# Optimization experiments

Hardware: AMD Instinct MI355X
Metric: run time of the kernel (lower is better)

Reference implementation:

```python
import jax, jax.numpy as jnp
import numpy as np

# dims: episodes E, steps S, comm length L, hidden H, rnn input IN, comm vocab OUT
E, S, L, H, IN, OUT = 64, 32, 32, 1024, 2048, 64
TAU = 2.0      # MTRNN leaky-integrator time constant
EPS = 1e-5     # BatchNorm eps


def setup_inputs() -> dict:
    key = jax.random.key(0)
    ks = jax.random.split(key, 16)
    def p(k, shape, scale=0.02):
        return jax.random.normal(k, shape, jnp.float32) * scale
    return {
        "h_w_action": jax.random.normal(ks[0], (E, S, IN), jnp.float32),
        # MTRNN cell
        "Wx": p(ks[1], (IN, H)), "bx": jnp.zeros((H,), jnp.float32),
        "Wh": p(ks[2], (H, H)), "bh": jnp.zeros((H,), jnp.float32),
        # Ted_Conv1d: 4 branches, kernels 1/3/5/7, each H//4 out channels (OIH layout)
        "w1": p(ks[3], (H // 4, H, 1)), "b1": jnp.zeros((H // 4,), jnp.float32),
        "w3": p(ks[4], (H // 4, H, 3)), "b3": jnp.zeros((H // 4,), jnp.float32),
        "w5": p(ks[5], (H // 4, H, 5)), "b5": jnp.zeros((H // 4,), jnp.float32),
        "w7": p(ks[6], (H // 4, H, 7)), "b7": jnp.zeros((H // 4,), jnp.float32),
        # BatchNorm1d affine
        "gamma": jnp.ones((H,), jnp.float32), "beta": jnp.zeros((H,), jnp.float32),
        # PReLU (single shared slope, torch default init 0.25)
        "prelu_a": jnp.array(0.25, jnp.float32),
        # output Linear
        "Wout": p(ks[7], (H, OUT)), "bout": jnp.zeros((OUT,), jnp.float32),
    }


def _conv(x, w, b):
    # x: [N, C, L], w: [O, I, k], 'same' padding for odd kernels
    pad = (w.shape[-1] - 1) // 2
    y = jax.lax.conv_general_dilated(x, w, (1,), [(pad, pad)],
                                     dimension_numbers=('NCH', 'OIH', 'NCH'))
    return y + b[None, :, None]


def reference(h_w_action, Wx, bx, Wh, bh, w1, b1, w3, b3, w5, b5, w7, b7,
              gamma, beta, prelu_a, Wout, bout):
    # MTRNN: same input every step; leaky integration h' = (1-1/tau)h + (1/tau)tanh(Wx x + Wh h)
    x_r = h_w_action @ Wx + bx                      # [E,S,H], constant across steps
    h0 = jnp.zeros((E, S, H), h_w_action.dtype)

    def step(h, _):
        h_new = (1.0 - 1.0 / TAU) * h + (1.0 / TAU) * jnp.tanh(x_r + h @ Wh + bh)
        return h_new, h_new

    _, hs = jax.lax.scan(step, h0, None, length=L)  # [L,E,S,H]
    hs = hs.transpose(1, 2, 0, 3).reshape(E * S, L, H)

    # multi-kernel conv over the comm-length axis
    xc = hs.transpose(0, 2, 1)                      # [N,H,L]
    y = jnp.concatenate([_conv(xc, w1, b1), _conv(xc, w3, b3),
                         _conv(xc, w5, b5), _conv(xc, w7, b7)], axis=1)  # [N,H,L]

    # BatchNorm1d (training-mode batch stats over N and L), affine
    mean = y.mean(axis=(0, 2), keepdims=True)
    var = y.var(axis=(0, 2), keepdims=True)
    y = (y - mean) * jax.lax.rsqrt(var + EPS) * gamma[None, :, None] + beta[None, :, None]

    # PReLU; Dropout is identity at eval
    y = jnp.where(y > 0, y, prelu_a * y)

    y = y.transpose(0, 2, 1).reshape(E, S, L, H)
    return y @ Wout + bout                          # [E,S,L,OUT]
```

## Files before the change

### kernel.cpp

```cpp
#include <hip/hip_runtime.h>
#include <cstdint>
#include <cmath>

#define DI __device__ __forceinline__


typedef __attribute__((ext_vector_type(8))) short bf16x8;
typedef __attribute__((ext_vector_type(4))) short s16x4;
typedef __attribute__((ext_vector_type(4))) float f32x4;

DI float bf2f(short u){
  union { unsigned int i; float f; } v; v.i = ((unsigned int)(unsigned short)u) << 16; return v.f;
}
DI short f2bf(float f){
  unsigned int x = __builtin_bit_cast(unsigned int, f);
  unsigned int r = (x + 0x7FFFu + ((x >> 16) & 1u)) >> 16;
  return (short)(unsigned short)r;
}
DI void gload16(const void* g, void* l){
  __builtin_amdgcn_global_load_lds(
      (const __attribute__((address_space(1))) unsigned int*)g,
      (__attribute__((address_space(3))) unsigned int*)l, 16, 0, 0);
}

template<int BM, int BN, int MODE>
__global__ __launch_bounds__(256)
void gemm_k(const short* __restrict__ A, long lda,
            const short* __restrict__ Bt, long ldb, int Ksteps,
            const float* __restrict__ bias,
            float* __restrict__ f32out,
            const float* __restrict__ f32in,
            short* __restrict__ bfout, int jj)
{
  constexpr int WTM = BM / 2, WTN = BN / 2;
  constexpr int FM = WTM / 16, FN = WTN / 16;
  __shared__ short As[BM * 64];
  __shared__ short Bs[BN * 64];
  const int tid = threadIdx.x;
  const int w = tid >> 6, l = tid & 63;
  const int wr = w >> 1, wc = w & 1;
  const int lr = l & 15, lk = (l >> 4) << 3;
  const int brow = blockIdx.x * BM;
  const int bcol = blockIdx.y * BN;

  int coff = 0, jout = 0;
  if constexpr (MODE == 2) {
    const int bb = bcol >> 7;
    const int dlt = (bb < 2) ? -3 : (bb < 6) ? -2 : (bb < 12) ? -1
                  : (bb < 20) ? 0 : (bb < 26) ? 1 : (bb < 30) ? 2 : 3;
    coff = (dlt == -3) ? 768 : (dlt == -2) ? 256 : (dlt == -1) ? -512
         : (dlt == 0) ? -1536 : (dlt == 1) ? -2304 : (dlt == 2) ? -2816 : -3072;
    jout = jj - dlt;
    if (jout < 0 || jout > 31) return;
  }

  f32x4 acc[FM][FN];
  #pragma unroll
  for (int i = 0; i < FM; i++)
    #pragma unroll
    for (int j = 0; j < FN; j++) {
      acc[i][j][0] = 0.f; acc[i][j][1] = 0.f; acc[i][j][2] = 0.f; acc[i][j][3] = 0.f;
    }

  for (int ks = 0; ks < Ksteps; ++ks) {
    const short* ab = A + (long)brow * lda + (long)ks * 64;
    #pragma unroll
    for (int it = 0; it < BM / 32; ++it) {
      int ci = it * 256 + tid;
      gload16(ab + (long)(ci >> 3) * lda + ((ci & 7) << 3),
              As + ((it * 256 + (w << 6)) << 3));
    }
    const short* bb2 = Bt + (long)bcol * ldb + (long)ks * 64;
    #pragma unroll
    for (int it = 0; it < BN / 32; ++it) {
      int ci = it * 256 + tid;
      gload16(bb2 + (long)(ci >> 3) * ldb + ((ci & 7) << 3),
              Bs + ((it * 256 + (w << 6)) << 3));
    }
    __syncthreads();
    #pragma unroll
    for (int kk = 0; kk < 64; kk += 32) {
      bf16x8 a[FM], b[FN];
      #pragma unroll
      for (int i = 0; i < FM; i++)
        a[i] = *(const bf16x8*)&As[(wr * WTM + i * 16 + lr) * 64 + kk + lk];
      #pragma unroll
      for (int j = 0; j < FN; j++)
        b[j] = *(const bf16x8*)&Bs[(wc * WTN + j * 16 + lr) * 64 + kk + lk];
      #pragma unroll
      for (int i = 0; i < FM; i++)
        #pragma unroll
        for (int j = 0; j < FN; j++)
          acc[i][j] = __builtin_amdgcn_mfma_f32_16x16x32_bf16(a[i], b[j], acc[i][j], 0, 0, 0);
    }
    __syncthreads();
  }

  const int rbase = brow + wr * WTM;
  const int cbase = bcol + wc * WTN;
  const int rl = (l >> 4) << 2;
  #pragma unroll
  for (int i = 0; i < FM; i++) {
    #pragma unroll
    for (int j = 0; j < FN; j++) {
      #pragma unroll
      for (int r = 0; r < 4; r++) {
        const int row = rbase + i * 16 + rl + r;
        const int col = cbase + j * 16 + lr;
        const float v = acc[i][j][r];
        if constexpr (MODE == 0) {
          f32out[(long)row * 1024 + col] = v + bias[col];
        } else if constexpr (MODE == 1) {
          const long idx = (long)row * 1024 + col;
          const float hn = 0.5f * f32out[idx] + 0.5f * tanhf(f32in[idx] + v + bias[col]);
          f32out[idx] = hn;
          bfout[idx] = f2bf(hn);
        } else if constexpr (MODE == 2) {
          short* yp = bfout + ((long)row * 32 + jout) * 1024 + (col + coff);
          *yp = f2bf(bf2f(*yp) + v);
        } else {
          f32out[(long)row * 64 + col] = v + bias[col];
        }
      }
    }
  }
}

__global__ void zero16(float4* __restrict__ p, long n)
{
  long i = (long)blockIdx.x * 256 + threadIdx.x;
  if (i < n) p[i] = float4{0.f, 0.f, 0.f, 0.f};
}

__global__ void cvt4_f32_bf16(const float* __restrict__ in, short* __restrict__ out, int n4)
{
  int i = blockIdx.x * 256 + threadIdx.x;
  if (i >= n4) return;
  float4 v = ((const float4*)in)[i];
  s16x4 o; o[0] = f2bf(v.x); o[1] = f2bf(v.y); o[2] = f2bf(v.z); o[3] = f2bf(v.w);
  ((s16x4*)out)[i] = o;
}

__global__ void transpose_f32_bf16(const float* __restrict__ in, short* __restrict__ out,
                                   int R, int C)
{
  __shared__ short tile[32][33];
  const int tx = threadIdx.x & 31, ty = threadIdx.x >> 5;
  const int c0 = blockIdx.x * 32, r0 = blockIdx.y * 32;
  #pragma unroll
  for (int i = 0; i < 32; i += 8)
    tile[ty + i][tx] = f2bf(in[(long)(r0 + ty + i) * C + (c0 + tx)]);
  __syncthreads();
  #pragma unroll
  for (int i = 0; i < 32; i += 8)
    out[(long)(c0 + ty + i) * R + (r0 + tx)] = tile[tx][ty + i];
}

__global__ void build_wpack(const float* __restrict__ w1, const float* __restrict__ w3,
                            const float* __restrict__ w5, const float* __restrict__ w7,
                            short* __restrict__ Wp)
{
  const int pc = blockIdx.x;
  int dlt, c;
  if      (pc < 256)  { dlt = -3; c = pc + 768; }
  else if (pc < 768)  { dlt = -2; c = pc + 256; }
  else if (pc < 1536) { dlt = -1; c = pc - 512; }
  else if (pc < 2560) { dlt = 0;  c = pc - 1536; }
  else if (pc < 3328) { dlt = 1;  c = pc - 2304; }
  else if (pc < 3840) { dlt = 2;  c = pc - 2816; }
  else                { dlt = 3;  c = pc - 3072; }
  const int b = c >> 8, kb = 2 * b + 1, t = dlt + b, oo = c & 255;
  const float* w = (b == 0) ? w1 : (b == 1) ? w3 : (b == 2) ? w5 : w7;
  short* dst = Wp + (long)pc * 1024;
  for (int i = threadIdx.x; i < 1024; i += 256)
    dst[i] = f2bf(w[((long)oo * 1024 + i) * kb + t]);
}

__global__ void bn_stats(const short* __restrict__ y, float* __restrict__ sum,
                         float* __restrict__ ssq)
{
  const int c0 = threadIdx.x * 4;
  float s0 = 0, s1 = 0, s2 = 0, s3 = 0, q0 = 0, q1 = 0, q2 = 0, q3 = 0;
  const long base = (long)blockIdx.x * 256;
  for (int r = 0; r < 256; ++r) {
    s16x4 v = *(const s16x4*)(y + (base + r) * 1024 + c0);
    float f0 = bf2f(v[0]), f1 = bf2f(v[1]), f2v = bf2f(v[2]), f3 = bf2f(v[3]);
    s0 += f0; s1 += f1; s2 += f2v; s3 += f3;
    q0 += f0 * f0; q1 += f1 * f1; q2 += f2v * f2v; q3 += f3 * f3;
  }
  atomicAdd(&sum[c0 + 0], s0); atomicAdd(&sum[c0 + 1], s1);
  atomicAdd(&sum[c0 + 2], s2); atomicAdd(&sum[c0 + 3], s3);
  atomicAdd(&ssq[c0 + 0], q0); atomicAdd(&ssq[c0 + 1], q1);
  atomicAdd(&ssq[c0 + 2], q2); atomicAdd(&ssq[c0 + 3], q3);
}

__global__ void bn_finalize(const float* __restrict__ bnsum, const float* __restrict__ bnss,
                            const float* __restrict__ gamma, const float* __restrict__ beta,
                            float* __restrict__ scale, float* __restrict__ shift)
{
  int c = blockIdx.x * 256 + threadIdx.x;
  const float inv = 1.f / 65536.f;
  float mean = bnsum[c] * inv;
  float var = bnss[c] * inv - mean * mean;
  float sc = gamma[c] * rsqrtf(var + 1e-5f);
  scale[c] = sc;
  shift[c] = beta[c] - mean * sc;
}

__global__ void bn_apply(short* __restrict__ y, const float* __restrict__ scale,
                         const float* __restrict__ shift, const float* __restrict__ aP)
{
  const float a = *aP;
  long i = (long)blockIdx.x * 256 + threadIdx.x;
  s16x4 v = ((s16x4*)y)[i];
  int c0 = (int)((i * 4) & 1023);
  #pragma unroll
  for (int j = 0; j < 4; ++j) {
    float f = bf2f(v[j]) * scale[c0 + j] + shift[c0 + j];
    f = f > 0.f ? f : a * f;
    v[j] = f2bf(f);
  }
  ((s16x4*)y)[i] = v;
}

extern "C" void kernel_launch(void* const* d_in, const int* in_sizes, int n_in,
                              void* d_out, int out_size, void* d_ws, size_t ws_size,
                              hipStream_t stream)
{
  const float* h_w_action = (const float*)d_in[0];
  const float* Wx   = (const float*)d_in[1];
  const float* bx   = (const float*)d_in[2];
  const float* Wh   = (const float*)d_in[3];
  const float* bh   = (const float*)d_in[4];
  const float* w1   = (const float*)d_in[5];
  const float* w3   = (const float*)d_in[7];
  const float* w5   = (const float*)d_in[9];
  const float* w7   = (const float*)d_in[11];
  const float* gamma = (const float*)d_in[13];
  const float* beta  = (const float*)d_in[14];
  const float* prelu = (const float*)d_in[15];
  const float* Wout  = (const float*)d_in[16];
  const float* bout  = (const float*)d_in[17];
  float* out = (float*)d_out;

  char* p = (char*)d_ws;
  auto alloc = [&](size_t bytes) -> char* {
    char* r = p; p += (bytes + 255) & ~(size_t)255; return r;
  };
  short* y     = (short*)alloc(65536L * 1024 * 2);
  float* xr    = (float*)alloc(2048L * 1024 * 4);
  float* hf    = (float*)alloc(2048L * 1024 * 4);
  short* hb0   = (short*)alloc(2048L * 1024 * 2);
  short* hb1   = (short*)alloc(2048L * 1024 * 2);
  short* A1    = (short*)alloc(2048L * 2048 * 2);
  short* WxT   = (short*)alloc(1024L * 2048 * 2);
  short* WhT   = (short*)alloc(1024L * 1024 * 2);
  short* Wp    = (short*)alloc(4096L * 1024 * 2);
  short* WoutT = (short*)alloc(64L * 1024 * 2);
  float* bnsum = (float*)alloc(1024 * 4);
  float* bnss  = (float*)alloc(1024 * 4);
  float* scal  = (float*)alloc(1024 * 4);
  float* shft  = (float*)alloc(1024 * 4);

  if ((size_t)(p - (char*)d_ws) > ws_size) return;

  zero16<<<32768, 256, 0, stream>>>((float4*)y, 65536L * 1024 * 2 / 16);
  zero16<<<2048, 256, 0, stream>>>((float4*)hf, 2048L * 1024 * 4 / 16);
  zero16<<<1024, 256, 0, stream>>>((float4*)hb0, 2048L * 1024 * 2 / 16);
  zero16<<<1, 256, 0, stream>>>((float4*)bnsum, 256);
  zero16<<<1, 256, 0, stream>>>((float4*)bnss, 256);

  cvt4_f32_bf16<<<4096, 256, 0, stream>>>(h_w_action, A1, 2048 * 2048 / 4);
  transpose_f32_bf16<<<dim3(32, 64), 256, 0, stream>>>(Wx, WxT, 2048, 1024);
  transpose_f32_bf16<<<dim3(32, 32), 256, 0, stream>>>(Wh, WhT, 1024, 1024);
  transpose_f32_bf16<<<dim3(2, 32), 256, 0, stream>>>(Wout, WoutT, 1024, 64);
  build_wpack<<<4096, 256, 0, stream>>>(w1, w3, w5, w7, Wp);

  gemm_k<128, 128, 0><<<dim3(16, 8), 256, 0, stream>>>(
      A1, 2048, WxT, 2048, 32, bx, xr, nullptr, nullptr, 0);

  short* hb[2] = {hb0, hb1};
  for (int s = 1; s <= 32; ++s) {
    gemm_k<64, 128, 1><<<dim3(32, 8), 256, 0, stream>>>(
        hb[(s - 1) & 1], 1024, WhT, 1024, 16, bh, hf, xr, hb[s & 1], 0);
    gemm_k<128, 128, 2><<<dim3(16, 32), 256, 0, stream>>>(
        hb[s & 1], 1024, Wp, 1024, 16, nullptr, nullptr, nullptr, y, s - 1);
  }

  bn_stats<<<256, 256, 0, stream>>>(y, bnsum, bnss);
  bn_finalize<<<4, 256, 0, stream>>>(bnsum, bnss, gamma, beta, scal, shft);
  bn_apply<<<65536, 256, 0, stream>>>(y, scal, shft, prelu);

  gemm_k<128, 64, 3><<<dim3(512, 1), 256, 0, stream>>>(
      y, 1024, WoutT, 1024, 16, bout, out, nullptr, nullptr, 0);
}
```

Baseline: 2.136 ms.

## Fuse BN apply and PReLU into output GEMM, retile GEMMs, precompute load pointers

Drops the separate bn_apply pass over the 128MB bf16 activation buffer. The output GEMM now applies the BatchNorm scale/shift and PReLU while staging A tiles into LDS, which saves a full read and write of y. It also increases bn_stats parallelism, shrinks the tiles of the input projection and recurrent GEMMs to launch more blocks, and hoists the global load pointer arithmetic out of the K loop. The fused kernel uses register loads for A instead of direct-to-LDS loads, which may add latency in the output GEMM.

```diff
diff --git a/kernel.cpp b/kernel.cpp
--- a/kernel.cpp
+++ b/kernel.cpp
@@ -34,6 +34,7 @@
 {
   constexpr int WTM = BM / 2, WTN = BN / 2;
   constexpr int FM = WTM / 16, FN = WTN / 16;
+  constexpr int AIT = BM / 32, BIT = BN / 32;
   __shared__ short As[BM * 64];
   __shared__ short Bs[BN * 64];
   const int tid = threadIdx.x;
@@ -62,20 +63,27 @@
       acc[i][j][0] = 0.f; acc[i][j][1] = 0.f; acc[i][j][2] = 0.f; acc[i][j][3] = 0.f;
     }
 
+  const short* ap[AIT];
+  const short* bp[BIT];
+  const int rsub = tid >> 3;
+  const int koff = (tid & 7) << 3;
+  #pragma unroll
+  for (int it = 0; it < AIT; ++it)
+    ap[it] = A + (long)(brow + it * 32 + rsub) * lda + koff;
+  #pragma unroll
+  for (int it = 0; it < BIT; ++it)
+    bp[it] = Bt + (long)(bcol + it * 32 + rsub) * ldb + koff;
+
   for (int ks = 0; ks < Ksteps; ++ks) {
-    const short* ab = A + (long)brow * lda + (long)ks * 64;
-    #pragma unroll
-    for (int it = 0; it < BM / 32; ++it) {
-      int ci = it * 256 + tid;
-      gload16(ab + (long)(ci >> 3) * lda + ((ci & 7) << 3),
-              As + ((it * 256 + (w << 6)) << 3));
-    }
-    const short* bb2 = Bt + (long)bcol * ldb + (long)ks * 64;
-    #pragma unroll
-    for (int it = 0; it < BN / 32; ++it) {
-      int ci = it * 256 + tid;
-      gload16(bb2 + (long)(ci >> 3) * ldb + ((ci & 7) << 3),
-              Bs + ((it * 256 + (w << 6)) << 3));
+    #pragma unroll
+    for (int it = 0; it < AIT; ++it) {
+      gload16(ap[it], As + ((it * 256 + (w << 6)) << 3));
+      ap[it] += 64;
+    }
+    #pragma unroll
+    for (int it = 0; it < BIT; ++it) {
+      gload16(bp[it], Bs + ((it * 256 + (w << 6)) << 3));
+      bp[it] += 64;
     }
     __syncthreads();
     #pragma unroll
@@ -126,6 +134,94 @@
   }
 }
 
+__global__ __launch_bounds__(256)
+void g5_bn(const short* __restrict__ y, const short* __restrict__ WoutT,
+           const float* __restrict__ scal, const float* __restrict__ shft,
+           const float* __restrict__ aP, const float* __restrict__ bout,
+           float* __restrict__ out)
+{
+  __shared__ short As[128 * 64];
+  __shared__ short Bs[64 * 64];
+  __shared__ float sS[1024], sB[1024];
+  const int tid = threadIdx.x;
+  const int w = tid >> 6, l = tid & 63;
+  const int wr = w >> 1, wc = w & 1;
+  const int lr = l & 15, lk = (l >> 4) << 3;
+  const int m0 = blockIdx.x * 128;
+  for (int i = tid; i < 1024; i += 256) { sS[i] = scal[i]; sB[i] = shft[i]; }
+  const float a = *aP;
+  __syncthreads();
+
+  f32x4 acc[4][2];
+  #pragma unroll
+  for (int i = 0; i < 4; i++)
+    #pragma unroll
+    for (int j = 0; j < 2; j++) {
+      acc[i][j][0] = 0.f; acc[i][j][1] = 0.f; acc[i][j][2] = 0.f; acc[i][j][3] = 0.f;
+    }
+
+  const int rsub = tid >> 3;
+  const int koff = (tid & 7) << 3;
+  const short* yp[4];
+  #pragma unroll
+  for (int it = 0; it < 4; ++it)
+    yp[it] = y + (long)(m0 + it * 32 + rsub) * 1024 + koff;
+  const short* bp[2];
+  #pragma unroll
+  for (int it = 0; it < 2; ++it)
+    bp[it] = WoutT + (long)(it * 32 + rsub) * 1024 + koff;
+
+  for (int ks = 0; ks < 16; ++ks) {
+    #pragma unroll
+    for (int it = 0; it < 2; ++it) {
+      gload16(bp[it], Bs + ((it * 256 + (w << 6)) << 3));
+      bp[it] += 64;
+    }
+    const int c0 = ks * 64 + koff;
+    #pragma unroll
+    for (int it = 0; it < 4; ++it) {
+      bf16x8 v = *(const bf16x8*)yp[it];
+      yp[it] += 64;
+      #pragma unroll
+      for (int e = 0; e < 8; ++e) {
+        float f = bf2f(v[e]) * sS[c0 + e] + sB[c0 + e];
+        v[e] = f2bf(f > 0.f ? f : a * f);
+      }
+      *(bf16x8*)(As + ((it * 256 + tid) << 3)) = v;
+    }
+    __syncthreads();
+    #pragma unroll
+    for (int kk = 0; kk < 64; kk += 32) {
+      bf16x8 af[4], bf_[2];
+      #pragma unroll
+      for (int i = 0; i < 4; i++)
+        af[i] = *(const bf16x8*)&As[(wr * 64 + i * 16 + lr) * 64 + kk + lk];
+      #pragma unroll
+      for (int j = 0; j < 2; j++)
+        bf_[j] = *(const bf16x8*)&Bs[(wc * 32 + j * 16 + lr) * 64 + kk + lk];
+      #pragma unroll
+      for (int i = 0; i < 4; i++)
+        #pragma unroll
+        for (int j = 0; j < 2; j++)
+          acc[i][j] = __builtin_amdgcn_mfma_f32_16x16x32_bf16(af[i], bf_[j], acc[i][j], 0, 0, 0);
+    }
+    __syncthreads();
+  }
+
+  const int rbase = m0 + wr * 64, cbase = wc * 32;
+  const int rl = (l >> 4) << 2;
+  #pragma unroll
+  for (int i = 0; i < 4; i++)
+    #pragma unroll
+    for (int j = 0; j < 2; j++)
+      #pragma unroll
+      for (int r = 0; r < 4; r++) {
+        const int row = rbase + i * 16 + rl + r;
+        const int col = cbase + j * 16 + lr;
+        out[(long)row * 64 + col] = acc[i][j][r] + bout[col];
+      }
+}
+
 __global__ void zero16(float4* __restrict__ p, long n)
 {
   long i = (long)blockIdx.x * 256 + threadIdx.x;
@@ -181,8 +277,8 @@
 {
   const int c0 = threadIdx.x * 4;
   float s0 = 0, s1 = 0, s2 = 0, s3 = 0, q0 = 0, q1 = 0, q2 = 0, q3 = 0;
-  const long base = (long)blockIdx.x * 256;
-  for (int r = 0; r < 256; ++r) {
+  const long base = (long)blockIdx.x * 32;
+  for (int r = 0; r < 32; ++r) {
     s16x4 v = *(const s16x4*)(y + (base + r) * 1024 + c0);
     float f0 = bf2f(v[0]), f1 = bf2f(v[1]), f2v = bf2f(v[2]), f3 = bf2f(v[3]);
     s0 += f0; s1 += f1; s2 += f2v; s3 += f3;
@@ -205,22 +301,6 @@
   float sc = gamma[c] * rsqrtf(var + 1e-5f);
   scale[c] = sc;
   shift[c] = beta[c] - mean * sc;
-}
-
-__global__ void bn_apply(short* __restrict__ y, const float* __restrict__ scale,
-                         const float* __restrict__ shift, const float* __restrict__ aP)
-{
-  const float a = *aP;
-  long i = (long)blockIdx.x * 256 + threadIdx.x;
-  s16x4 v = ((s16x4*)y)[i];
-  int c0 = (int)((i * 4) & 1023);
-  #pragma unroll
-  for (int j = 0; j < 4; ++j) {
-    float f = bf2f(v[j]) * scale[c0 + j] + shift[c0 + j];
-    f = f > 0.f ? f : a * f;
-    v[j] = f2bf(f);
-  }
-  ((s16x4*)y)[i] = v;
 }
 
 extern "C" void kernel_launch(void* const* d_in, const int* in_sizes, int n_in,
@@ -276,21 +356,19 @@
   transpose_f32_bf16<<<dim3(2, 32), 256, 0, stream>>>(Wout, WoutT, 1024, 64);
   build_wpack<<<4096, 256, 0, stream>>>(w1, w3, w5, w7, Wp);
 
-  gemm_k<128, 128, 0><<<dim3(16, 8), 256, 0, stream>>>(
+  gemm_k<64, 128, 0><<<dim3(32, 8), 256, 0, stream>>>(
       A1, 2048, WxT, 2048, 32, bx, xr, nullptr, nullptr, 0);
 
   short* hb[2] = {hb0, hb1};
   for (int s = 1; s <= 32; ++s) {
-    gemm_k<64, 128, 1><<<dim3(32, 8), 256, 0, stream>>>(
+    gemm_k<64, 64, 1><<<dim3(32, 16), 256, 0, stream>>>(
         hb[(s - 1) & 1], 1024, WhT, 1024, 16, bh, hf, xr, hb[s & 1], 0);
     gemm_k<128, 128, 2><<<dim3(16, 32), 256, 0, stream>>>(
         hb[s & 1], 1024, Wp, 1024, 16, nullptr, nullptr, nullptr, y, s - 1);
   }
 
-  bn_stats<<<256, 256, 0, stream>>>(y, bnsum, bnss);
+  bn_stats<<<2048, 256, 0, stream>>>(y, bnsum, bnss);
   bn_finalize<<<4, 256, 0, stream>>>(bnsum, bnss, gamma, beta, scal, shft);
-  bn_apply<<<65536, 256, 0, stream>>>(y, scal, shft, prelu);
-
-  gemm_k<128, 64, 3><<<dim3(512, 1), 256, 0, stream>>>(
-      y, 1024, WoutT, 1024, 16, bout, out, nullptr, nullptr, 0);
-}
+
+  g5_bn<<<dim3(512, 1), 256, 0, stream>>>(y, WoutT, scal, shft, prelu, bout, out);
+}
```

New measurement: 2.044 ms. 4.3% less time.
